# Optimization experiments

Hardware: AMD Instinct MI355X
Metric: run time of the kernel (lower is better)

Reference implementation:

```python
import jax, jax.numpy as jnp
import numpy as np

E = 8        # num_experts (material buckets)
L1 = 3072    # input dim
L2 = 15
L3 = 32
RF = 32      # ROUTER_FEATURES_PER_PERSPECTIVE
B = 16384
AUX_ALPHA = 0.01
Z_ALPHA = 0.001
LOAD_FLOOR = 0.05
LOAD_CAP = 0.5
PROBE_ALPHA = 0.01
PROBE_TAU = 1.0
PROBE_THRESH = 0.05
TEACHER_ALPHA = 0.0   # initial value of _teacher_alpha buffer
SCORE_SCALE = 600.0
SQ_SCALE = 255.0 / 256.0


def setup_inputs() -> dict:
    key = jax.random.key(0)
    ks = jax.random.split(key, 12)
    x = jax.random.uniform(ks[0], (B, L1), dtype=jnp.float32)
    ls_indices = jax.random.randint(ks[1], (B,), 0, E)
    psqt = jax.random.normal(ks[2], (B,), dtype=jnp.float32)
    score_target = jax.random.normal(ks[3], (B,), dtype=jnp.float32)
    router_w = 0.1 * jax.random.normal(ks[4], (E, 2 * RF), dtype=jnp.float32)
    router_b = jnp.zeros((E,), dtype=jnp.float32)
    # effective (coalesced) expert params, per _expert_params view
    w1 = jax.random.normal(ks[5], (E, L2 + 1, L1), dtype=jnp.float32) / np.sqrt(L1)
    b1 = 0.01 * jax.random.normal(ks[6], (E, L2 + 1), dtype=jnp.float32)
    w2 = jax.random.normal(ks[7], (E, L3, 2 * L2), dtype=jnp.float32) / np.sqrt(2 * L2)
    b2 = 0.01 * jax.random.normal(ks[8], (E, L3), dtype=jnp.float32)
    w3 = jax.random.normal(ks[9], (E, 1, L3), dtype=jnp.float32) / np.sqrt(L3)
    b3 = jnp.zeros((E, 1), dtype=jnp.float32)  # output bias zeroed in __init__
    return {"x": x, "ls_indices": ls_indices, "psqt": psqt,
            "score_target": score_target, "router_w": router_w,
            "router_b": router_b, "w1": w1, "b1": b1, "w2": w2, "b2": b2,
            "w3": w3, "b3": b3}


def _forward(x, psqt, score_target, router_w, router_b, w1, b1, w2, b2, w3, b3, ls_indices):
    half = L1 // 2
    router_in = jnp.concatenate([x[:, :RF], x[:, half:half + RF]], axis=1)  # [B, 64]
    gate_logits = router_in @ router_w.T + router_b                          # [B, E]
    logp = jax.nn.log_softmax(gate_logits, axis=-1)
    gate_probs = jnp.exp(logp)
    expert_indices = jnp.argmax(gate_logits, axis=-1)                        # [B]

    teacher_ce = -jnp.mean(jnp.take_along_axis(logp, ls_indices[:, None], axis=1))
    frac = jnp.bincount(expert_indices, length=E).astype(gate_probs.dtype) / gate_probs.shape[0]
    avg_gate = gate_probs.mean(axis=0)
    load = avg_gate + jax.lax.stop_gradient(frac - avg_gate)
    floor_loss = jnp.mean(jnp.square(jnp.maximum(LOAD_FLOOR - load, 0.0)))
    cap_loss = jnp.mean(jnp.square(jnp.maximum(load - LOAD_CAP, 0.0)))
    aux_loss = floor_loss + cap_loss
    z_loss = jnp.mean(jnp.square(jax.nn.logsumexp(gate_logits, axis=-1)))

    # ---- all-experts stacked MLP (fusion target) ----
    l1c = jnp.einsum('bi,eoi->beo', x, w1) + b1          # [B, E, L2+1]
    a, a_skip = l1c[..., :L2], l1c[..., L2:]              # [B,E,L2], [B,E,1]
    h = jnp.clip(jnp.concatenate([a * a * SQ_SCALE, a], axis=-1), 0.0, 1.0)  # [B,E,2*L2]
    l2x = jnp.clip(jnp.einsum('bei,eoi->beo', h, w2) + b2, 0.0, 1.0)         # [B,E,L3]
    all_out = jnp.einsum('bei,eoi->beo', l2x, w3) + b3 + a_skip              # [B,E,1]

    # ---- probe loss ----
    probe_weight = PROBE_ALPHA * max(PROBE_THRESH - TEACHER_ALPHA, 0.0) / max(PROBE_THRESH, 1e-9)
    expert_out = (all_out[..., 0] + psqt[:, None]) * SCORE_SCALE             # [B, E]
    err = jnp.square(expert_out - score_target[:, None])
    err = err - err.min(axis=1, keepdims=True)
    pt = jax.nn.softmax(-jax.lax.stop_gradient(err) / PROBE_TAU, axis=-1)
    log_pt = jnp.log(jnp.maximum(pt, 1e-30))
    probe_loss = jnp.mean(jnp.sum(pt * (log_pt - logp), axis=-1))            # kl_div batchmean

    router_loss = (AUX_ALPHA * aux_loss + Z_ALPHA * z_loss
                   + TEACHER_ALPHA * teacher_ce + probe_weight * probe_loss)

    l3x = jnp.take_along_axis(all_out, expert_indices[:, None, None], axis=1)[:, 0, :]  # [B, 1]
    gp = jnp.take_along_axis(gate_probs, expert_indices[:, None], axis=1)               # [B, 1]
    l3x = l3x * (1.0 + gp - jax.lax.stop_gradient(gp))  # straight-through (training mode)
    return l3x, router_loss


def reference(x, ls_indices, psqt, score_target, router_w, router_b, w1, b1, w2, b2, w3, b3):
    return _forward(x, psqt, score_target, router_w, router_b, w1, b1, w2, b2, w3, b3, ls_indices)
```

## Files before the change

### kernel.cpp

```cpp
#include <hip/hip_runtime.h>
#include <math.h>

#define BATCH 16384
#define K_DIM 3072
#define NOUT  128
#define NEXP  8

typedef float  f32x4  __attribute__((ext_vector_type(4)));
typedef __bf16 bf16x8 __attribute__((ext_vector_type(8)));
typedef unsigned int u32x4 __attribute__((ext_vector_type(4)));
typedef unsigned int u32x2 __attribute__((ext_vector_type(2)));

__device__ __forceinline__ unsigned short f2bf(float f) {
  union { float f; unsigned u; } v; v.f = f;
  unsigned u = v.u + 0x7fffu + ((v.u >> 16) & 1u);
  return (unsigned short)(u >> 16);
}

__global__ void cvt_w1_kernel(const float* __restrict__ w1, unsigned short* __restrict__ o) {
  int i = blockIdx.x * 256 + threadIdx.x;
  f32x4 v = ((const f32x4*)w1)[i];
  u32x2 p = { (unsigned)f2bf(v.x) | ((unsigned)f2bf(v.y) << 16),
              (unsigned)f2bf(v.z) | ((unsigned)f2bf(v.w) << 16) };
  ((u32x2*)o)[i] = p;
}

__global__ void router_kernel(const float* __restrict__ x, const float* __restrict__ rw,
                              const float* __restrict__ rb, float* __restrict__ logp,
                              int* __restrict__ eidx, float* __restrict__ accs) {
  __shared__ float rws[512];
  __shared__ float rbs[8];
  __shared__ int   hist[8];
  __shared__ float zred[4];
  const int tid = threadIdx.x;
  if (tid < 8) { hist[tid] = 0; rbs[tid] = rb[tid]; }
  for (int i = tid; i < 512; i += 256) rws[i] = rw[i];
  __syncthreads();

  const int b = blockIdx.x * 256 + tid;
  const float* xr = x + (size_t)b * K_DIM;
  double l[8];
#pragma unroll
  for (int e = 0; e < 8; ++e) l[e] = (double)rbs[e];
  for (int c = 0; c < 32; ++c) {
    double xv = (double)xr[c];
#pragma unroll
    for (int e = 0; e < 8; ++e) l[e] = fma(xv, (double)rws[e * 64 + c], l[e]);
  }
  for (int c = 0; c < 32; ++c) {
    double xv = (double)xr[1536 + c];
#pragma unroll
    for (int e = 0; e < 8; ++e) l[e] = fma(xv, (double)rws[e * 64 + 32 + c], l[e]);
  }
  double best = l[0]; int bi = 0;
#pragma unroll
  for (int e = 1; e < 8; ++e) if (l[e] > best) { best = l[e]; bi = e; }
  double s = 0.0;
#pragma unroll
  for (int e = 0; e < 8; ++e) s += exp(l[e] - best);
  double lse = best + log(s);
#pragma unroll
  for (int e = 0; e < 8; ++e) logp[(size_t)b * 8 + e] = (float)(l[e] - lse);
  eidx[b] = bi;
  atomicAdd(&hist[bi], 1);

  float z = (float)(lse * lse);
  for (int m = 1; m < 64; m <<= 1) z += __shfl_xor(z, m);
  if ((tid & 63) == 0) zred[tid >> 6] = z;
  __syncthreads();
  if (tid == 0) atomicAdd(&accs[8], zred[0] + zred[1] + zred[2] + zred[3]);
  if (tid < 8) atomicAdd(&accs[tid], (float)hist[tid]);
}

__global__ __launch_bounds__(256, 2) void moe_main_kernel(
    const float* __restrict__ x, const unsigned short* __restrict__ w1bf,
    const float* __restrict__ b1, const float* __restrict__ w2,
    const float* __restrict__ b2, const float* __restrict__ w3,
    const float* __restrict__ b3, const float* __restrict__ psqt,
    const float* __restrict__ st, const float* __restrict__ logp,
    const int* __restrict__ eidx, float* __restrict__ out,
    float* __restrict__ accs) {
  __shared__ __align__(16) unsigned short stage[32 * 72 + 128 * 72];
  __shared__ __align__(16) float w2s[8 * 964];
  __shared__ float b1s[128], b2s[256], w3s[256], b3s[8], wred[4];

  const int tid = threadIdx.x;
  const int bm  = blockIdx.x;
  unsigned short* xs  = stage;
  unsigned short* wsd = stage + 32 * 72;
  float* Cl = (float*)stage;

  for (int i = tid; i < 7680; i += 256) {
    int e = i / 960; int r = i - e * 960; int o = r / 30; int ii = r - o * 30;
    w2s[e * 964 + ii * 32 + o] = w2[i];
  }
  if (tid < 128) b1s[tid] = b1[tid];
  b2s[tid] = b2[tid];
  w3s[tid] = w3[tid];
  if (tid < 8) b3s[tid] = b3[tid];

  const int lane = tid & 63, wv = tid >> 6;
  const int l16 = lane & 15, lq = lane >> 4;
  const int rt = wv & 1;
  const int cb = (wv >> 1) * 4;

  const int xr0 = tid >> 4, xc4 = tid & 15;
  const float* gx0 = x + (size_t)(bm * 32 + xr0) * K_DIM + xc4 * 4;
  const float* gx1 = gx0 + (size_t)16 * K_DIM;
  const int xo0 = xr0 * 72 + xc4 * 4;
  const int xo1 = (xr0 + 16) * 72 + xc4 * 4;
  const int wr0 = tid >> 3, wc8 = tid & 7;
  const unsigned short* gw = w1bf + (size_t)wr0 * K_DIM + wc8 * 8;
  const int wo0 = wr0 * 72 + wc8 * 8;

  f32x4 acc[4];
#pragma unroll
  for (int c = 0; c < 4; ++c) acc[c] = (f32x4){0.f, 0.f, 0.f, 0.f};

  f32x4 xv0 = *(const f32x4*)gx0;
  f32x4 xv1 = *(const f32x4*)gx1;
  u32x4 wv0 = *(const u32x4*)(gw);
  u32x4 wv1 = *(const u32x4*)(gw + 32 * K_DIM);
  u32x4 wv2 = *(const u32x4*)(gw + 64 * K_DIM);
  u32x4 wv3 = *(const u32x4*)(gw + 96 * K_DIM);

  const int abase = (rt * 16 + l16) * 72 + lq * 8;
  const int bbase = (cb * 16 + l16) * 72 + lq * 8;

  for (int kt = 0; kt < 48; ++kt) {
    __syncthreads();
    {
      u32x2 p0 = { (unsigned)f2bf(xv0.x) | ((unsigned)f2bf(xv0.y) << 16),
                   (unsigned)f2bf(xv0.z) | ((unsigned)f2bf(xv0.w) << 16) };
      *(u32x2*)&xs[xo0] = p0;
      u32x2 p1 = { (unsigned)f2bf(xv1.x) | ((unsigned)f2bf(xv1.y) << 16),
                   (unsigned)f2bf(xv1.z) | ((unsigned)f2bf(xv1.w) << 16) };
      *(u32x2*)&xs[xo1] = p1;
      *(u32x4*)&wsd[wo0]           = wv0;
      *(u32x4*)&wsd[wo0 + 32 * 72] = wv1;
      *(u32x4*)&wsd[wo0 + 64 * 72] = wv2;
      *(u32x4*)&wsd[wo0 + 96 * 72] = wv3;
    }
    __syncthreads();
    if (kt < 47) {
      gx0 += 64; gx1 += 64;
      xv0 = *(const f32x4*)gx0;
      xv1 = *(const f32x4*)gx1;
      const unsigned short* g = gw + (kt + 1) * 64;
      wv0 = *(const u32x4*)(g);
      wv1 = *(const u32x4*)(g + 32 * K_DIM);
      wv2 = *(const u32x4*)(g + 64 * K_DIM);
      wv3 = *(const u32x4*)(g + 96 * K_DIM);
    }
#pragma unroll
    for (int ks = 0; ks < 2; ++ks) {
      bf16x8 af = *(const bf16x8*)&xs[abase + ks * 32];
#pragma unroll
      for (int c = 0; c < 4; ++c) {
        bf16x8 bfv = *(const bf16x8*)&wsd[bbase + c * 16 * 72 + ks * 32];
        acc[c] = __builtin_amdgcn_mfma_f32_16x16x32_bf16(af, bfv, acc[c], 0, 0, 0);
      }
    }
  }

  __syncthreads();
#pragma unroll
  for (int c = 0; c < 4; ++c)
#pragma unroll
    for (int r = 0; r < 4; ++r)
      Cl[(rt * 16 + lq * 4 + r) * 132 + (cb + c) * 16 + l16] = acc[c][r];
  __syncthreads();

  const int bl = tid >> 3, e = tid & 7;
  const int bg = bm * 32 + bl;

  float a[16];
#pragma unroll
  for (int j = 0; j < 16; ++j) a[j] = Cl[bl * 132 + e * 16 + j] + b1s[e * 16 + j];

  float h[30];
#pragma unroll
  for (int j = 0; j < 15; ++j) {
    float v = a[j];
    h[j]      = fminf(fmaxf(v * v * (255.0f / 256.0f), 0.f), 1.f);
    h[15 + j] = fminf(fmaxf(v, 0.f), 1.f);
  }

  float acc2[32];
#pragma unroll
  for (int o = 0; o < 32; ++o) acc2[o] = b2s[e * 32 + o];
  const f32x4* wrow = (const f32x4*)&w2s[e * 964];
#pragma unroll
  for (int i = 0; i < 30; ++i) {
    float hv = h[i];
#pragma unroll
    for (int o4 = 0; o4 < 8; ++o4) {
      f32x4 wq = wrow[i * 8 + o4];
      acc2[o4 * 4 + 0] += hv * wq.x;
      acc2[o4 * 4 + 1] += hv * wq.y;
      acc2[o4 * 4 + 2] += hv * wq.z;
      acc2[o4 * 4 + 3] += hv * wq.w;
    }
  }

  float outv = b3s[e] + a[15];
#pragma unroll
  for (int o = 0; o < 32; ++o) {
    float l2v = fminf(fmaxf(acc2[o], 0.f), 1.f);
    outv += l2v * w3s[e * 32 + o];
  }

  float eo  = (outv + psqt[bg]) * 600.0f;
  float dd  = eo - st[bg];
  float err = dd * dd;
  float mn = err;
  mn = fminf(mn, __shfl_xor(mn, 1));
  mn = fminf(mn, __shfl_xor(mn, 2));
  mn = fminf(mn, __shfl_xor(mn, 4));
  float wexp = expf(-(err - mn));
  float ssum = wexp;
  ssum += __shfl_xor(ssum, 1); ssum += __shfl_xor(ssum, 2); ssum += __shfl_xor(ssum, 4);
  float pt  = wexp / ssum;
  float lpt = logf(fmaxf(pt, 1e-30f));
  float term = pt * (lpt - logp[(size_t)bg * 8 + e]);
  term += __shfl_xor(term, 1); term += __shfl_xor(term, 2); term += __shfl_xor(term, 4);
  float c1 = (e == 0) ? term : 0.f;
  c1 += __shfl_xor(c1, 8); c1 += __shfl_xor(c1, 16); c1 += __shfl_xor(c1, 32);
  if (lane == 0) wred[wv] = c1;

  if (e == eidx[bg]) out[bg] = outv;

  __syncthreads();
  if (tid == 0) atomicAdd(&accs[9], wred[0] + wred[1] + wred[2] + wred[3]);
}

__global__ void finalize_kernel(const float* __restrict__ accs, float* __restrict__ out) {
  if (threadIdx.x == 0) {
    float fsum = 0.f;
    for (int e = 0; e < 8; ++e) {
      float frac = accs[e] * (1.0f / 16384.0f);
      float f = fmaxf(0.05f - frac, 0.f);
      float c = fmaxf(frac - 0.5f, 0.f);
      fsum += f * f + c * c;
    }
    float aux   = fsum * 0.125f;
    float z     = accs[8] * (1.0f / 16384.0f);
    float probe = accs[9] * (1.0f / 16384.0f);
    out[BATCH] = 0.01f * aux + 0.001f * z + 0.01f * probe;
  }
}

extern "C" void kernel_launch(void* const* d_in, const int* in_sizes, int n_in,
                              void* d_out, int out_size, void* d_ws, size_t ws_size,
                              hipStream_t stream) {
  const float* x    = (const float*)d_in[0];
  const float* psqt = (const float*)d_in[2];
  const float* st   = (const float*)d_in[3];
  const float* rw   = (const float*)d_in[4];
  const float* rb   = (const float*)d_in[5];
  const float* w1   = (const float*)d_in[6];
  const float* b1   = (const float*)d_in[7];
  const float* w2   = (const float*)d_in[8];
  const float* b2   = (const float*)d_in[9];
  const float* w3   = (const float*)d_in[10];
  const float* b3   = (const float*)d_in[11];
  float* out = (float*)d_out;

  unsigned short* w1bf = (unsigned short*)d_ws;
  float* logp = (float*)((char*)d_ws + 786432);
  int*   eidx = (int*)((char*)d_ws + 786432 + 524288);
  float* accs = (float*)((char*)d_ws + 786432 + 524288 + 65536);

  hipMemsetAsync(accs, 0, 16 * sizeof(float), stream);
  cvt_w1_kernel<<<384, 256, 0, stream>>>(w1, w1bf);
  router_kernel<<<64, 256, 0, stream>>>(x, rw, rb, logp, eidx, accs);
  moe_main_kernel<<<512, 256, 0, stream>>>(x, w1bf, b1, w2, b2, w3, b3,
                                           psqt, st, logp, eidx, out, accs);
  finalize_kernel<<<1, 1, 0, stream>>>(accs, out);
}
```

Before: 339.9 us.

## Fuse router into main MoE kernel and load GEMM fragments directly to registers

```diff
diff --git a/kernel.cpp b/kernel.cpp
--- a/kernel.cpp
+++ b/kernel.cpp
@@ -17,7 +17,20 @@
   return (unsigned short)(u >> 16);
 }
 
-__global__ void cvt_w1_kernel(const float* __restrict__ w1, unsigned short* __restrict__ o) {
+__device__ __forceinline__ bf16x8 asbf(u32x4 v) {
+  union { u32x4 u; bf16x8 b; } c; c.u = v; return c.b;
+}
+
+__device__ __forceinline__ bf16x8 cvt8(f32x4 lo, f32x4 hi) {
+  bf16x8 r;
+  r[0] = (__bf16)lo[0]; r[1] = (__bf16)lo[1]; r[2] = (__bf16)lo[2]; r[3] = (__bf16)lo[3];
+  r[4] = (__bf16)hi[0]; r[5] = (__bf16)hi[1]; r[6] = (__bf16)hi[2]; r[7] = (__bf16)hi[3];
+  return r;
+}
+
+__global__ void cvt_w1_kernel(const float* __restrict__ w1, unsigned short* __restrict__ o,
+                              float* __restrict__ accs) {
+  if (blockIdx.x == 0 && threadIdx.x < 16) accs[threadIdx.x] = 0.f;
   int i = blockIdx.x * 256 + threadIdx.x;
   f32x4 v = ((const f32x4*)w1)[i];
   u32x2 p = { (unsigned)f2bf(v.x) | ((unsigned)f2bf(v.y) << 16),
@@ -25,154 +38,127 @@
   ((u32x2*)o)[i] = p;
 }
 
-__global__ void router_kernel(const float* __restrict__ x, const float* __restrict__ rw,
-                              const float* __restrict__ rb, float* __restrict__ logp,
-                              int* __restrict__ eidx, float* __restrict__ accs) {
-  __shared__ float rws[512];
-  __shared__ float rbs[8];
-  __shared__ int   hist[8];
-  __shared__ float zred[4];
-  const int tid = threadIdx.x;
-  if (tid < 8) { hist[tid] = 0; rbs[tid] = rb[tid]; }
-  for (int i = tid; i < 512; i += 256) rws[i] = rw[i];
-  __syncthreads();
-
-  const int b = blockIdx.x * 256 + tid;
-  const float* xr = x + (size_t)b * K_DIM;
-  double l[8];
-#pragma unroll
-  for (int e = 0; e < 8; ++e) l[e] = (double)rbs[e];
-  for (int c = 0; c < 32; ++c) {
-    double xv = (double)xr[c];
-#pragma unroll
-    for (int e = 0; e < 8; ++e) l[e] = fma(xv, (double)rws[e * 64 + c], l[e]);
-  }
-  for (int c = 0; c < 32; ++c) {
-    double xv = (double)xr[1536 + c];
-#pragma unroll
-    for (int e = 0; e < 8; ++e) l[e] = fma(xv, (double)rws[e * 64 + 32 + c], l[e]);
-  }
-  double best = l[0]; int bi = 0;
-#pragma unroll
-  for (int e = 1; e < 8; ++e) if (l[e] > best) { best = l[e]; bi = e; }
-  double s = 0.0;
-#pragma unroll
-  for (int e = 0; e < 8; ++e) s += exp(l[e] - best);
-  double lse = best + log(s);
-#pragma unroll
-  for (int e = 0; e < 8; ++e) logp[(size_t)b * 8 + e] = (float)(l[e] - lse);
-  eidx[b] = bi;
-  atomicAdd(&hist[bi], 1);
-
-  float z = (float)(lse * lse);
-  for (int m = 1; m < 64; m <<= 1) z += __shfl_xor(z, m);
-  if ((tid & 63) == 0) zred[tid >> 6] = z;
-  __syncthreads();
-  if (tid == 0) atomicAdd(&accs[8], zred[0] + zred[1] + zred[2] + zred[3]);
-  if (tid < 8) atomicAdd(&accs[tid], (float)hist[tid]);
-}
-
 __global__ __launch_bounds__(256, 2) void moe_main_kernel(
     const float* __restrict__ x, const unsigned short* __restrict__ w1bf,
     const float* __restrict__ b1, const float* __restrict__ w2,
     const float* __restrict__ b2, const float* __restrict__ w3,
     const float* __restrict__ b3, const float* __restrict__ psqt,
-    const float* __restrict__ st, const float* __restrict__ logp,
-    const int* __restrict__ eidx, float* __restrict__ out,
+    const float* __restrict__ st, const float* __restrict__ rw,
+    const float* __restrict__ rb, float* __restrict__ out,
     float* __restrict__ accs) {
-  __shared__ __align__(16) unsigned short stage[32 * 72 + 128 * 72];
+  __shared__ __align__(16) float Cl[32 * 132];
   __shared__ __align__(16) float w2s[8 * 964];
-  __shared__ float b1s[128], b2s[256], w3s[256], b3s[8], wred[4];
+  __shared__ float b1s[128], b2s[256], w3s[256], b3s[8];
+  __shared__ float rws[8 * 65];
+  __shared__ float wred[4], zred[4];
+  __shared__ int   hist[8];
 
   const int tid = threadIdx.x;
   const int bm  = blockIdx.x;
-  unsigned short* xs  = stage;
-  unsigned short* wsd = stage + 32 * 72;
-  float* Cl = (float*)stage;
 
   for (int i = tid; i < 7680; i += 256) {
     int e = i / 960; int r = i - e * 960; int o = r / 30; int ii = r - o * 30;
     w2s[e * 964 + ii * 32 + o] = w2[i];
   }
+  for (int i = tid; i < 512; i += 256) rws[(i >> 6) * 65 + (i & 63)] = rw[i];
   if (tid < 128) b1s[tid] = b1[tid];
   b2s[tid] = b2[tid];
   w3s[tid] = w3[tid];
-  if (tid < 8) b3s[tid] = b3[tid];
+  if (tid < 8) { b3s[tid] = b3[tid]; hist[tid] = 0; }
+  __syncthreads();
 
   const int lane = tid & 63, wv = tid >> 6;
   const int l16 = lane & 15, lq = lane >> 4;
   const int rt = wv & 1;
   const int cb = (wv >> 1) * 4;
 
-  const int xr0 = tid >> 4, xc4 = tid & 15;
-  const float* gx0 = x + (size_t)(bm * 32 + xr0) * K_DIM + xc4 * 4;
-  const float* gx1 = gx0 + (size_t)16 * K_DIM;
-  const int xo0 = xr0 * 72 + xc4 * 4;
-  const int xo1 = (xr0 + 16) * 72 + xc4 * 4;
-  const int wr0 = tid >> 3, wc8 = tid & 7;
-  const unsigned short* gw = w1bf + (size_t)wr0 * K_DIM + wc8 * 8;
-  const int wo0 = wr0 * 72 + wc8 * 8;
+  const float*          pA = x    + (size_t)(bm * 32 + rt * 16 + l16) * K_DIM + lq * 8;
+  const unsigned short* pB = w1bf + (size_t)(cb * 16 + l16) * K_DIM + lq * 8;
+
+  f32x4 aR[2][4];
+  u32x4 bR[2][8];
+
+#define LOADT(S, KT) do {                                        \
+    const float* pa_ = pA + (KT) * 64;                           \
+    aR[S][0] = *(const f32x4*)(pa_);                             \
+    aR[S][1] = *(const f32x4*)(pa_ + 4);                         \
+    aR[S][2] = *(const f32x4*)(pa_ + 32);                        \
+    aR[S][3] = *(const f32x4*)(pa_ + 36);                        \
+    const unsigned short* pb_ = pB + (KT) * 64;                  \
+    bR[S][0] = *(const u32x4*)(pb_);                             \
+    bR[S][1] = *(const u32x4*)(pb_ + 32);                        \
+    bR[S][2] = *(const u32x4*)(pb_ + 16 * K_DIM);                \
+    bR[S][3] = *(const u32x4*)(pb_ + 16 * K_DIM + 32);           \
+    bR[S][4] = *(const u32x4*)(pb_ + 32 * K_DIM);                \
+    bR[S][5] = *(const u32x4*)(pb_ + 32 * K_DIM + 32);           \
+    bR[S][6] = *(const u32x4*)(pb_ + 48 * K_DIM);                \
+    bR[S][7] = *(const u32x4*)(pb_ + 48 * K_DIM + 32);           \
+  } while (0)
+
+#define COMPUTE(S) do {                                                              \
+    bf16x8 af0 = cvt8(aR[S][0], aR[S][1]);                                           \
+    bf16x8 af1 = cvt8(aR[S][2], aR[S][3]);                                           \
+    _Pragma("unroll")                                                                \
+    for (int c = 0; c < 4; ++c)                                                      \
+      acc[c] = __builtin_amdgcn_mfma_f32_16x16x32_bf16(af0, asbf(bR[S][c * 2 + 0]),  \
+                                                       acc[c], 0, 0, 0);             \
+    _Pragma("unroll")                                                                \
+    for (int c = 0; c < 4; ++c)                                                      \
+      acc[c] = __builtin_amdgcn_mfma_f32_16x16x32_bf16(af1, asbf(bR[S][c * 2 + 1]),  \
+                                                       acc[c], 0, 0, 0);             \
+  } while (0)
+
+  LOADT(0, 0);
+
+  const int bl = tid >> 3, e = tid & 7;
+  const int bg = bm * 32 + bl;
+  const float* xrow = x + (size_t)bg * K_DIM;
+  double lr = (double)rb[e];
+#pragma unroll
+  for (int c = 0; c < 32; ++c)
+    lr = fma((double)xrow[c], (double)rws[e * 65 + c], lr);
+#pragma unroll
+  for (int c = 0; c < 32; ++c)
+    lr = fma((double)xrow[1536 + c], (double)rws[e * 65 + 32 + c], lr);
+
+  double mx = lr; int mi = e;
+#pragma unroll
+  for (int m = 1; m < 8; m <<= 1) {
+    double ov = __shfl_xor(mx, m);
+    int    oi = __shfl_xor(mi, m);
+    if (ov > mx || (ov == mx && oi < mi)) { mx = ov; mi = oi; }
+  }
+  double ssum = exp(lr - mx);
+#pragma unroll
+  for (int m = 1; m < 8; m <<= 1) ssum += __shfl_xor(ssum, m);
+  const double lse = mx + log(ssum);
+  const float  logp_self = (float)(lr - lse);
+  const int    rowEidx   = mi;
+
+  if (e == 0) atomicAdd(&hist[rowEidx], 1);
+  float zc = (e == 0) ? (float)(lse * lse) : 0.f;
+#pragma unroll
+  for (int m = 1; m < 64; m <<= 1) zc += __shfl_xor(zc, m);
+  if (lane == 0) zred[wv] = zc;
 
   f32x4 acc[4];
 #pragma unroll
   for (int c = 0; c < 4; ++c) acc[c] = (f32x4){0.f, 0.f, 0.f, 0.f};
 
-  f32x4 xv0 = *(const f32x4*)gx0;
-  f32x4 xv1 = *(const f32x4*)gx1;
-  u32x4 wv0 = *(const u32x4*)(gw);
-  u32x4 wv1 = *(const u32x4*)(gw + 32 * K_DIM);
-  u32x4 wv2 = *(const u32x4*)(gw + 64 * K_DIM);
-  u32x4 wv3 = *(const u32x4*)(gw + 96 * K_DIM);
-
-  const int abase = (rt * 16 + l16) * 72 + lq * 8;
-  const int bbase = (cb * 16 + l16) * 72 + lq * 8;
-
-  for (int kt = 0; kt < 48; ++kt) {
-    __syncthreads();
-    {
-      u32x2 p0 = { (unsigned)f2bf(xv0.x) | ((unsigned)f2bf(xv0.y) << 16),
-                   (unsigned)f2bf(xv0.z) | ((unsigned)f2bf(xv0.w) << 16) };
-      *(u32x2*)&xs[xo0] = p0;
-      u32x2 p1 = { (unsigned)f2bf(xv1.x) | ((unsigned)f2bf(xv1.y) << 16),
-                   (unsigned)f2bf(xv1.z) | ((unsigned)f2bf(xv1.w) << 16) };
-      *(u32x2*)&xs[xo1] = p1;
-      *(u32x4*)&wsd[wo0]           = wv0;
-      *(u32x4*)&wsd[wo0 + 32 * 72] = wv1;
-      *(u32x4*)&wsd[wo0 + 64 * 72] = wv2;
-      *(u32x4*)&wsd[wo0 + 96 * 72] = wv3;
-    }
-    __syncthreads();
-    if (kt < 47) {
-      gx0 += 64; gx1 += 64;
-      xv0 = *(const f32x4*)gx0;
-      xv1 = *(const f32x4*)gx1;
-      const unsigned short* g = gw + (kt + 1) * 64;
-      wv0 = *(const u32x4*)(g);
-      wv1 = *(const u32x4*)(g + 32 * K_DIM);
-      wv2 = *(const u32x4*)(g + 64 * K_DIM);
-      wv3 = *(const u32x4*)(g + 96 * K_DIM);
-    }
-#pragma unroll
-    for (int ks = 0; ks < 2; ++ks) {
-      bf16x8 af = *(const bf16x8*)&xs[abase + ks * 32];
-#pragma unroll
-      for (int c = 0; c < 4; ++c) {
-        bf16x8 bfv = *(const bf16x8*)&wsd[bbase + c * 16 * 72 + ks * 32];
-        acc[c] = __builtin_amdgcn_mfma_f32_16x16x32_bf16(af, bfv, acc[c], 0, 0, 0);
-      }
-    }
-  }
-
-  __syncthreads();
+#pragma unroll 1
+  for (int kt = 0; kt < 48; kt += 2) {
+    LOADT(1, kt + 1);
+    COMPUTE(0);
+    if (kt + 2 < 48) LOADT(0, kt + 2);
+    COMPUTE(1);
+  }
+
 #pragma unroll
   for (int c = 0; c < 4; ++c)
 #pragma unroll
     for (int r = 0; r < 4; ++r)
       Cl[(rt * 16 + lq * 4 + r) * 132 + (cb + c) * 16 + l16] = acc[c][r];
   __syncthreads();
-
-  const int bl = tid >> 3, e = tid & 7;
-  const int bg = bm * 32 + bl;
 
   float a[16];
 #pragma unroll
@@ -218,20 +204,26 @@
   mn = fminf(mn, __shfl_xor(mn, 2));
   mn = fminf(mn, __shfl_xor(mn, 4));
   float wexp = expf(-(err - mn));
-  float ssum = wexp;
-  ssum += __shfl_xor(ssum, 1); ssum += __shfl_xor(ssum, 2); ssum += __shfl_xor(ssum, 4);
-  float pt  = wexp / ssum;
+  float ss = wexp;
+  ss += __shfl_xor(ss, 1); ss += __shfl_xor(ss, 2); ss += __shfl_xor(ss, 4);
+  float pt  = wexp / ss;
   float lpt = logf(fmaxf(pt, 1e-30f));
-  float term = pt * (lpt - logp[(size_t)bg * 8 + e]);
+  float term = pt * (lpt - logp_self);
   term += __shfl_xor(term, 1); term += __shfl_xor(term, 2); term += __shfl_xor(term, 4);
   float c1 = (e == 0) ? term : 0.f;
   c1 += __shfl_xor(c1, 8); c1 += __shfl_xor(c1, 16); c1 += __shfl_xor(c1, 32);
   if (lane == 0) wred[wv] = c1;
 
-  if (e == eidx[bg]) out[bg] = outv;
+  if (e == rowEidx) out[bg] = outv;
 
   __syncthreads();
-  if (tid == 0) atomicAdd(&accs[9], wred[0] + wred[1] + wred[2] + wred[3]);
+  if (tid == 0) {
+    atomicAdd(&accs[8], zred[0] + zred[1] + zred[2] + zred[3]);
+    atomicAdd(&accs[9], wred[0] + wred[1] + wred[2] + wred[3]);
+  }
+  if (tid < 8) atomicAdd(&accs[tid], (float)hist[tid]);
+#undef LOADT
+#undef COMPUTE
 }
 
 __global__ void finalize_kernel(const float* __restrict__ accs, float* __restrict__ out) {
@@ -267,14 +259,10 @@
   float* out = (float*)d_out;
 
   unsigned short* w1bf = (unsigned short*)d_ws;
-  float* logp = (float*)((char*)d_ws + 786432);
-  int*   eidx = (int*)((char*)d_ws + 786432 + 524288);
-  float* accs = (float*)((char*)d_ws + 786432 + 524288 + 65536);
-
-  hipMemsetAsync(accs, 0, 16 * sizeof(float), stream);
-  cvt_w1_kernel<<<384, 256, 0, stream>>>(w1, w1bf);
-  router_kernel<<<64, 256, 0, stream>>>(x, rw, rb, logp, eidx, accs);
+  float* accs = (float*)((char*)d_ws + 786432);
+
+  cvt_w1_kernel<<<384, 256, 0, stream>>>(w1, w1bf, accs);
   moe_main_kernel<<<512, 256, 0, stream>>>(x, w1bf, b1, w2, b2, w3, b3,
-                                           psqt, st, logp, eidx, out, accs);
+                                           psqt, st, rw, rb, out, accs);
   finalize_kernel<<<1, 1, 0, stream>>>(accs, out);
 }
```

After: 387.9 us. 1.14x slower.
